# Kernel tuning notes

Hardware: AMD Instinct MI355X
Metric: run time of the kernel (lower is better)

## Reference

```python
import jax, jax.numpy as jnp
import numpy as np

B, S, D = 4, 2048, 1024

def setup_inputs() -> dict:
    key = jax.random.key(0)
    k0, k1, k2, k3 = jax.random.split(key, 4)
    scale = 1.0 / np.sqrt(D)
    return {
        "x": jax.random.normal(k0, (B, S, D), dtype=jnp.float32),
        "Wq": jax.random.normal(k1, (D, D), dtype=jnp.float32) * scale,
        "Wk": jax.random.normal(k2, (D, D), dtype=jnp.float32) * scale,
        "Wv": jax.random.normal(k3, (D, D), dtype=jnp.float32) * scale,
    }

def reference(x, Wq, Wk, Wv):
    # x: [B,S,D]; Wq/Wk/Wv: [D_in, D_out] (equivalent to torch Linear weight transposed)
    q = jnp.einsum('bsd,de->bse', x, Wq)
    k = jnp.einsum('bsd,de->bse', x, Wk)
    v = jnp.einsum('bsd,de->bse', x, Wv)
    d_out = k.shape[-1]
    scores = jnp.einsum('bqe,bke->bqk', q, k)  # [B,S,S]
    S_ = scores.shape[-1]
    causal = jnp.tril(jnp.ones((S_, S_), dtype=bool))  # True = keep
    # masked_fill before scaling == after scaling (-inf invariant under positive scale)
    scores = jnp.where(causal, scores, -jnp.inf)
    attn = jax.nn.softmax(scores / jnp.sqrt(jnp.asarray(d_out, scores.dtype)), axis=-1)
    # dropout p=0.0 -> identity
    return jnp.einsum('bqk,bke->bqe', attn, v)
```

## Files before the change

### kernel.cpp

```cpp
#include <hip/hip_runtime.h>

#define B_  4
#define S_  2048
#define D_  1024
#define N_  (B_*S_)
#define SCALE 0.03125f
#define NEGINF (-3.0e38f)

typedef unsigned short u16;
typedef __attribute__((ext_vector_type(8))) short short8;
typedef __attribute__((ext_vector_type(4))) float floatx4;

__device__ __forceinline__ u16 f2bf(float f) {
    unsigned int u = __float_as_uint(f);
    u += 0x7FFFu + ((u >> 16) & 1u);
    return (u16)(u >> 16);
}
__device__ __forceinline__ float bf2f(u16 h) {
    return __uint_as_float((unsigned int)h << 16);
}

__device__ __forceinline__ void gl_lds16(const void* g, void* l) {
    __builtin_amdgcn_global_load_lds(
        (const __attribute__((address_space(1))) unsigned int*)g,
        (__attribute__((address_space(3))) unsigned int*)l, 16, 0, 0);
}

__device__ __forceinline__ int xcd_chunk(int bid, int nwg) {
    return (bid & 7) * (nwg >> 3) + (bid >> 3);
}

__global__ __launch_bounds__(256) void cast_fused(const float* __restrict__ x,
                                                  const float* __restrict__ Wq, const float* __restrict__ Wk,
                                                  const float* __restrict__ Wv,
                                                  u16* __restrict__ xb, u16* __restrict__ Wqb,
                                                  u16* __restrict__ Wkb, u16* __restrict__ Wvt) {
    __shared__ float t[32][33];
    const int blk = blockIdx.x;
    if (blk < 5120) {
        const float* src; u16* dst; size_t i;
        if (blk < 4096)      { src = x;  dst = xb;  i = (size_t)blk * 2048; }
        else if (blk < 4608) { src = Wq; dst = Wqb; i = (size_t)(blk - 4096) * 2048; }
        else                 { src = Wk; dst = Wkb; i = (size_t)(blk - 4608) * 2048; }
        i += (size_t)threadIdx.x * 8;
        float4 a = *(const float4*)&src[i];
        float4 b = *(const float4*)&src[i + 4];
        short8 o;
        o[0]=f2bf(a.x); o[1]=f2bf(a.y); o[2]=f2bf(a.z); o[3]=f2bf(a.w);
        o[4]=f2bf(b.x); o[5]=f2bf(b.y); o[6]=f2bf(b.z); o[7]=f2bf(b.w);
        *(short8*)&dst[i] = o;
    } else {
        const int tb = blk - 5120;
        const int c = threadIdx.x & 31, r0 = threadIdx.x >> 5;
        const int i0 = (tb >> 5) * 32, j0 = (tb & 31) * 32;
#pragma unroll
        for (int rr = 0; rr < 4; ++rr)
            t[r0 + rr * 8][c] = Wv[(size_t)(i0 + r0 + rr * 8) * D_ + j0 + c];
        __syncthreads();
#pragma unroll
        for (int rr = 0; rr < 4; ++rr)
            Wvt[(size_t)(j0 + r0 + rr * 8) * D_ + i0 + c] = f2bf(t[c][r0 + rr * 8]);
    }
}


__device__ __forceinline__ void mfma_nt_128(const u16* __restrict__ A, int lda,
                                            const u16* __restrict__ Bp, int ldb,
                                            int m0, int n0, int kext,
                                            u16* Sh, floatx4 acc[4][4])
{
    const int tid  = threadIdx.x;
    const int lane = tid & 63;
    const int lr   = lane & 15, quad = lane >> 4;
    const int wm   = ((tid >> 6) & 1) * 64, wn = (tid >> 7) * 64;
    const int nt   = kext >> 6;

    auto stage8 = [&](int t) {
#pragma unroll
        for (int h = 0; h < 8; ++h) {
            const int kk = h >> 2, mat = (h >> 1) & 1, half = h & 1;
            const int idx = tid * 8;
            const int row = half * 64 + (idx >> 5);
            const int s   = (idx & 31) >> 3;
            const int gk  = (t << 6) + kk * 32 + ((s ^ ((row >> 1) & 3)) << 3);
            u16* dst = Sh + (t & 1) * 16384 + mat * 8192 + kk * 4096 + half * 2048 + idx;
            const u16* src = mat ? &Bp[(size_t)(n0 + row) * ldb + gk]
                                 : &A [(size_t)(m0 + row) * lda + gk];
            gl_lds16(src, dst);
        }
    };

    stage8(0);
    for (int t = 0; t < nt; ++t) {
        asm volatile("s_waitcnt vmcnt(0)" ::: "memory");
        __builtin_amdgcn_s_barrier();
        if (t + 1 < nt) stage8(t + 1);
        const u16* buf = Sh + (t & 1) * 16384;
#pragma unroll
        for (int kk = 0; kk < 2; ++kk) {
            short8 af[4], bf[4];
#pragma unroll
            for (int i = 0; i < 4; ++i) {
                const int ar = wm + i * 16 + lr;
                af[i] = *(const short8*)&buf[kk * 4096 + ar * 32 + ((quad ^ ((ar >> 1) & 3)) << 3)];
                const int br = wn + i * 16 + lr;
                bf[i] = *(const short8*)&buf[8192 + kk * 4096 + br * 32 + ((quad ^ ((br >> 1) & 3)) << 3)];
            }
            __builtin_amdgcn_s_setprio(1);
#pragma unroll
            for (int i = 0; i < 4; ++i)
#pragma unroll
                for (int j = 0; j < 4; ++j)
                    acc[i][j] = __builtin_amdgcn_mfma_f32_16x16x32_bf16(af[i], bf[j], acc[i][j], 0, 0, 0);
            __builtin_amdgcn_s_setprio(0);
        }
    }
}

#define EPI_VARS                                              \
    const int lane = threadIdx.x & 63;                        \
    const int lr = lane & 15, quad = lane >> 4;               \
    const int wm = ((threadIdx.x >> 6) & 1) * 64, wn = (threadIdx.x >> 7) * 64;

__device__ __forceinline__ void mfma_nt_128w8(const u16* __restrict__ A, int lda,
                                              const u16* __restrict__ Bp, int ldb,
                                              int m0, int n0, int kext,
                                              u16* Sh, floatx4 acc[2][4])
{
    const int tid  = threadIdx.x;
    const int lane = tid & 63;
    const int lr   = lane & 15, quad = lane >> 4;
    const int wid  = tid >> 6;
    const int wm   = (wid >> 1) * 32;
    const int wn   = (wid & 1) * 64;
    const int nt   = kext >> 6;

    auto stage4 = [&](int t) {
#pragma unroll
        for (int h = 0; h < 4; ++h) {
            const int kk = h >> 1, mat = h & 1;
            const int idx = tid * 8;
            const int row = idx >> 5;
            const int s   = (idx & 31) >> 3;
            const int gk  = (t << 6) + kk * 32 + ((s ^ ((row >> 1) & 3)) << 3);
            u16* dst = Sh + (t & 1) * 16384 + mat * 8192 + kk * 4096 + idx;
            const u16* src = mat ? &Bp[(size_t)(n0 + row) * ldb + gk]
                                 : &A [(size_t)(m0 + row) * lda + gk];
            gl_lds16(src, dst);
        }
    };

    stage4(0);
    for (int t = 0; t < nt; ++t) {
        asm volatile("s_waitcnt vmcnt(0)" ::: "memory");
        __builtin_amdgcn_s_barrier();
        if (t + 1 < nt) stage4(t + 1);
        const u16* buf = Sh + (t & 1) * 16384;
#pragma unroll
        for (int kk = 0; kk < 2; ++kk) {
            short8 af[2], bf[4];
#pragma unroll
            for (int i = 0; i < 2; ++i) {
                const int ar = wm + i * 16 + lr;
                af[i] = *(const short8*)&buf[kk * 4096 + ar * 32 + ((quad ^ ((ar >> 1) & 3)) << 3)];
            }
#pragma unroll
            for (int j = 0; j < 4; ++j) {
                const int br = wn + j * 16 + lr;
                bf[j] = *(const short8*)&buf[8192 + kk * 4096 + br * 32 + ((quad ^ ((br >> 1) & 3)) << 3)];
            }
            __builtin_amdgcn_s_setprio(1);
#pragma unroll
            for (int i = 0; i < 2; ++i)
#pragma unroll
                for (int j = 0; j < 4; ++j)
                    acc[i][j] = __builtin_amdgcn_mfma_f32_16x16x32_bf16(af[i], bf[j], acc[i][j], 0, 0, 0);
            __builtin_amdgcn_s_setprio(0);
        }
    }
}

__device__ __forceinline__ void mfma_nt_256(const u16* __restrict__ A, int lda,
                                            const u16* __restrict__ Bp, int ldb,
                                            int m0, int n0, int kext,
                                            u16* Sh, floatx4 acc[8][4])
{
    const int tid  = threadIdx.x;
    const int lane = tid & 63;
    const int lr   = lane & 15, quad = lane >> 4;
    const int wr   = (tid >> 8) & 1, wc = (tid >> 6) & 3;
    const int nt   = kext >> 6;

    auto stage8 = [&](int t) {
#pragma unroll
        for (int h = 0; h < 8; ++h) {
            const int kk = h >> 2, mat = (h >> 1) & 1, half = h & 1;
            const int idx = tid * 8;
            const int row = half * 128 + (idx >> 5);
            const int s   = (idx & 31) >> 3;
            const int gk  = (t << 6) + kk * 32 + ((s ^ ((row >> 1) & 3)) << 3);
            u16* dst = Sh + (t & 1) * 32768 + mat * 16384 + kk * 8192 + half * 4096 + idx;
            const u16* src = mat ? &Bp[(size_t)(n0 + row) * ldb + gk]
                                 : &A [(size_t)(m0 + row) * lda + gk];
            gl_lds16(src, dst);
        }
    };

    stage8(0);
    for (int t = 0; t < nt; ++t) {
        asm volatile("s_waitcnt vmcnt(0)" ::: "memory");
        __builtin_amdgcn_s_barrier();
        if (t + 1 < nt) stage8(t + 1);
        const u16* buf = Sh + (t & 1) * 32768;
#pragma unroll
        for (int kk = 0; kk < 2; ++kk) {
            short8 af[8], bf[4];
#pragma unroll
            for (int i = 0; i < 8; ++i) {
                const int ar = wr * 128 + i * 16 + lr;
                af[i] = *(const short8*)&buf[kk * 8192 + ar * 32 + ((quad ^ ((ar >> 1) & 3)) << 3)];
            }
#pragma unroll
            for (int j = 0; j < 4; ++j) {
                const int br = wc * 64 + j * 16 + lr;
                bf[j] = *(const short8*)&buf[16384 + kk * 8192 + br * 32 + ((quad ^ ((br >> 1) & 3)) << 3)];
            }
            __builtin_amdgcn_s_setprio(1);
#pragma unroll
            for (int i = 0; i < 8; ++i)
#pragma unroll
                for (int j = 0; j < 4; ++j)
                    acc[i][j] = __builtin_amdgcn_mfma_f32_16x16x32_bf16(af[i], bf[j], acc[i][j], 0, 0, 0);
            __builtin_amdgcn_s_setprio(0);
        }
    }
}

#define EPI256_VARS                                           \
    const int lane = threadIdx.x & 63;                        \
    const int lr = lane & 15, quad = lane >> 4;               \
    const int wr = (threadIdx.x >> 8) & 1, wc = (threadIdx.x >> 6) & 3;

__global__ __launch_bounds__(256) void mt_mfma(const u16* __restrict__ Wkb, const u16* __restrict__ Wqb,
                                               u16* __restrict__ Mt)
{
    __shared__ u16 Sh[32768];
    const int m0 = blockIdx.y * 128, n0 = blockIdx.x * 128;
    floatx4 acc[4][4];
#pragma unroll
    for (int i = 0; i < 4; ++i)
#pragma unroll
        for (int j = 0; j < 4; ++j) acc[i][j] = (floatx4){0.f, 0.f, 0.f, 0.f};
    mfma_nt_128(Wkb, D_, Wqb, D_, m0, n0, D_, Sh, acc);

    EPI_VARS
#pragma unroll
    for (int i = 0; i < 4; ++i)
#pragma unroll
        for (int j = 0; j < 4; ++j)
#pragma unroll
            for (int r = 0; r < 4; ++r)
                Mt[(size_t)(m0 + wm + i * 16 + quad * 4 + r) * D_ + n0 + wn + j * 16 + lr] = f2bf(acc[i][j][r]);
}

__global__ __launch_bounds__(512, 2) void yv_mfma(const u16* __restrict__ xb, const u16* __restrict__ Mt,
                                                  const u16* __restrict__ Wvt,
                                                  u16* __restrict__ Y, u16* __restrict__ Vt)
{
    __shared__ u16 Sh[65536];
    const int lid = xcd_chunk(blockIdx.x, 256);
    floatx4 acc[8][4];
#pragma unroll
    for (int i = 0; i < 8; ++i)
#pragma unroll
        for (int j = 0; j < 4; ++j) acc[i][j] = (floatx4){0.f, 0.f, 0.f, 0.f};

    if (lid < 128) {
        const int m0 = (lid >> 2) * 256, n0 = (lid & 3) * 256;
        mfma_nt_256(xb, D_, Mt, D_, m0, n0, D_, Sh, acc);
        EPI256_VARS
#pragma unroll
        for (int i = 0; i < 8; ++i)
#pragma unroll
            for (int j = 0; j < 4; ++j)
#pragma unroll
                for (int r = 0; r < 4; ++r)
                    Y[(size_t)(m0 + wr * 128 + i * 16 + quad * 4 + r) * D_ + n0 + wc * 64 + j * 16 + lr]
                        = f2bf(acc[i][j][r]);
    } else {
        const int v = lid - 128;
        const int b = v >> 5;
        const int mloc = ((v >> 2) & 7) * 256;
        const int n0 = (v & 3) * 256;
        const int m0 = b * S_ + mloc;
        u16* Vb = Vt + (size_t)b * D_ * S_;
        mfma_nt_256(xb, D_, Wvt, D_, m0, n0, D_, Sh, acc);
        EPI256_VARS
#pragma unroll
        for (int i = 0; i < 8; ++i)
#pragma unroll
            for (int j = 0; j < 4; ++j) {
                const int ee = n0 + wc * 64 + j * 16 + lr;
                const int s4 = mloc + wr * 128 + i * 16 + quad * 4;
                ushort4 o;
                o.x = f2bf(acc[i][j][0]); o.y = f2bf(acc[i][j][1]);
                o.z = f2bf(acc[i][j][2]); o.w = f2bf(acc[i][j][3]);
                *(ushort4*)&Vb[(size_t)ee * S_ + s4] = o;
            }
    }
}

__global__ __launch_bounds__(512, 2) void scores_mfma(const u16* __restrict__ Y, const u16* __restrict__ xb,
                                                      u16* __restrict__ Sc)
{
    __shared__ u16 Sh[65536];
    const int lid = xcd_chunk(blockIdx.x, 144);
    const int b = lid / 36;
    const int t = lid - b * 36;
    int qt = 0;
    while ((qt + 1) * (qt + 2) / 2 <= t) ++qt;
    const int kt = t - qt * (qt + 1) / 2;

    const u16* A  = Y  + (size_t)b * S_ * D_;
    const u16* Bp = xb + (size_t)b * S_ * D_;
    u16* Sb = Sc + (size_t)b * S_ * S_;
    const int m0 = qt * 256, n0 = kt * 256;
    floatx4 acc[8][4];
#pragma unroll
    for (int i = 0; i < 8; ++i)
#pragma unroll
        for (int j = 0; j < 4; ++j) acc[i][j] = (floatx4){0.f, 0.f, 0.f, 0.f};
    mfma_nt_256(A, D_, Bp, D_, m0, n0, D_, Sh, acc);

    EPI256_VARS
#pragma unroll
    for (int i = 0; i < 8; ++i)
#pragma unroll
        for (int r = 0; r < 4; ++r) {
            const int grow = m0 + wr * 128 + i * 16 + quad * 4 + r;
#pragma unroll
            for (int j = 0; j < 4; ++j) {
                const int gcol = n0 + wc * 64 + j * 16 + lr;
                const float v = (gcol <= grow) ? acc[i][j][r] * SCALE : NEGINF;
                Sb[(size_t)grow * S_ + gcol] = f2bf(v);
            }
        }
}

__global__ __launch_bounds__(256) void softmax_k(const u16* __restrict__ Sc, u16* __restrict__ P)
{
    const int row = blockIdx.x * 4 + (threadIdx.x >> 6);
    const int lane = threadIdx.x & 63;
    const int b = row >> 11, q = row & (S_ - 1);
    const int L = ((q >> 7) + 1) << 7;
    const u16* rp = Sc + ((size_t)b * S_ + q) * S_;
    u16* pp = P + ((size_t)b * S_ + q) * S_;

    float f[4][8];
    float lmax = -3.4e38f;
#pragma unroll
    for (int c = 0; c < 4; ++c) {
        const int i = c * 512 + lane * 8;
        if (i < L) {
            short8 v = *(const short8*)&rp[i];
#pragma unroll
            for (int k = 0; k < 8; ++k) { f[c][k] = bf2f((u16)v[k]); lmax = fmaxf(lmax, f[c][k]); }
        }
    }
#pragma unroll
    for (int off = 32; off; off >>= 1) lmax = fmaxf(lmax, __shfl_xor(lmax, off, 64));

    float lsum = 0.f;
#pragma unroll
    for (int c = 0; c < 4; ++c) {
        const int i = c * 512 + lane * 8;
        if (i < L) {
#pragma unroll
            for (int k = 0; k < 8; ++k) { f[c][k] = __expf(f[c][k] - lmax); lsum += f[c][k]; }
        }
    }
#pragma unroll
    for (int off = 32; off; off >>= 1) lsum += __shfl_xor(lsum, off, 64);
    const float inv = 1.0f / lsum;

#pragma unroll
    for (int c = 0; c < 4; ++c) {
        const int i = c * 512 + lane * 8;
        if (i < L) {
            short8 o;
#pragma unroll
            for (int k = 0; k < 8; ++k) o[k] = (short)f2bf(f[c][k] * inv);
            *(short8*)&pp[i] = o;
        }
    }
}

__device__ __forceinline__ void pv_epi(floatx4 acc[2][4], int b, int m0, int n0, float* __restrict__ O)
{
    const int lane = threadIdx.x & 63;
    const int lr = lane & 15, quad = lane >> 4;
    const int wid = threadIdx.x >> 6;
    const int wm = (wid >> 1) * 32, wn = (wid & 1) * 64;
#pragma unroll
    for (int i = 0; i < 2; ++i)
#pragma unroll
        for (int r = 0; r < 4; ++r) {
            const int grow = m0 + wm + i * 16 + quad * 4 + r;
#pragma unroll
            for (int j = 0; j < 4; ++j)
                O[((size_t)b * S_ + grow) * D_ + n0 + wn + j * 16 + lr] = acc[i][j][r];
        }
}

__global__ __launch_bounds__(512, 2) void pv_mfma(const u16* __restrict__ P, const u16* __restrict__ Vt,
                                                  float* __restrict__ O)
{
    __shared__ u16 Sh[32768];
    const int lid = xcd_chunk(blockIdx.x, 256);
    const int b  = lid >> 6;
    const int et = (lid >> 3) & 7;
    const int pr = lid & 7;
    const int n0 = et * 128;
    const u16* A  = P  + (size_t)b * S_ * S_;
    const u16* Bp = Vt + (size_t)b * D_ * S_;

    floatx4 acc[2][4];
    const int qtA = pr, qtB = 15 - pr;

#pragma unroll
    for (int i = 0; i < 2; ++i)
#pragma unroll
        for (int j = 0; j < 4; ++j) acc[i][j] = (floatx4){0.f, 0.f, 0.f, 0.f};
    mfma_nt_128w8(A, S_, Bp, S_, qtA * 128, n0, (qtA + 1) * 128, Sh, acc);
    pv_epi(acc, b, qtA * 128, n0, O);

#pragma unroll
    for (int i = 0; i < 2; ++i)
#pragma unroll
        for (int j = 0; j < 4; ++j) acc[i][j] = (floatx4){0.f, 0.f, 0.f, 0.f};
    mfma_nt_128w8(A, S_, Bp, S_, qtB * 128, n0, (qtB + 1) * 128, Sh, acc);
    pv_epi(acc, b, qtB * 128, n0, O);
}

extern "C" void kernel_launch(void* const* d_in, const int* in_sizes, int n_in,
                              void* d_out, int out_size, void* d_ws, size_t ws_size,
                              hipStream_t stream) {
    const float* x  = (const float*)d_in[0];
    const float* Wq = (const float*)d_in[1];
    const float* Wk = (const float*)d_in[2];
    const float* Wv = (const float*)d_in[3];
    float* out = (float*)d_out;
    char* w = (char*)d_ws;

    u16* xb  = (u16*)(w);
    u16* Wqb = (u16*)(w + 16777216);
    u16* Wkb = (u16*)(w + 18874368);
    u16* Wvt = (u16*)(w + 20971520);
    u16* Mt  = (u16*)(w + 23068672);
    u16* Y   = (u16*)(w + 25165824);
    u16* Vt  = (u16*)(w + 41943040);
    u16* Sc  = (u16*)(w + 58720256);
    u16* P   = (u16*)(w + 92274688);

    cast_fused <<<dim3(6144),   256, 0, stream>>>(x, Wq, Wk, Wv, xb, Wqb, Wkb, Wvt);
    mt_mfma    <<<dim3(8, 8),   256, 0, stream>>>(Wkb, Wqb, Mt);
    yv_mfma    <<<dim3(256),    512, 0, stream>>>(xb, Mt, Wvt, Y, Vt);
    scores_mfma<<<dim3(144),    512, 0, stream>>>(Y, xb, Sc);
    softmax_k  <<<dim3(N_/4),   256, 0, stream>>>(Sc, P);
    pv_mfma    <<<dim3(256),    512, 0, stream>>>(P, Vt, out);
}
```

Before: 211.0 us.

## Interleave per-slice global-to-LDS prefetch with MFMA half-tiles in 256x256 NT GEMM

Restructures the 256-wide NT GEMM main loop into a finer-grained ping-pong schedule. The next tile's loads are split into four A/B k-slices issued between half-tile MFMA phases, and partial vmcnt waits replace the full drain at each iteration. A-fragment registers are halved by processing the 8 row-fragments in two groups of four. The goal is to overlap global-to-LDS traffic with matrix math and cut register pressure, at the cost of many more barriers per iteration and fragile waitcnt accounting.

```diff
diff --git a/kernel.cpp b/kernel.cpp
--- a/kernel.cpp
+++ b/kernel.cpp
@@ -191,47 +191,77 @@
     const int wr   = (tid >> 8) & 1, wc = (tid >> 6) & 3;
     const int nt   = kext >> 6;
 
-    auto stage8 = [&](int t) {
-#pragma unroll
-        for (int h = 0; h < 8; ++h) {
-            const int kk = h >> 2, mat = (h >> 1) & 1, half = h & 1;
-            const int idx = tid * 8;
-            const int row = half * 128 + (idx >> 5);
+    auto stage = [&](int t, int mat, int kk) {
+#pragma unroll
+        for (int pass = 0; pass < 2; ++pass) {
+            const int idx = pass * 4096 + tid * 8;
+            const int row = idx >> 5;
             const int s   = (idx & 31) >> 3;
             const int gk  = (t << 6) + kk * 32 + ((s ^ ((row >> 1) & 3)) << 3);
-            u16* dst = Sh + (t & 1) * 32768 + mat * 16384 + kk * 8192 + half * 4096 + idx;
+            u16* dst = Sh + (t & 1) * 32768 + mat * 16384 + kk * 8192 + idx;
             const u16* src = mat ? &Bp[(size_t)(n0 + row) * ldb + gk]
                                  : &A [(size_t)(m0 + row) * lda + gk];
             gl_lds16(src, dst);
         }
     };
 
-    stage8(0);
+    stage(0, 0, 0); stage(0, 1, 0); stage(0, 0, 1); stage(0, 1, 1);
+    asm volatile("s_waitcnt vmcnt(4)" ::: "memory");
+    __builtin_amdgcn_s_barrier();
+
     for (int t = 0; t < nt; ++t) {
-        asm volatile("s_waitcnt vmcnt(0)" ::: "memory");
-        __builtin_amdgcn_s_barrier();
-        if (t + 1 < nt) stage8(t + 1);
         const u16* buf = Sh + (t & 1) * 32768;
+        const bool pf = (t + 1 < nt);
+        short8 af[4], bf[4];
+
 #pragma unroll
         for (int kk = 0; kk < 2; ++kk) {
-            short8 af[8], bf[4];
-#pragma unroll
-            for (int i = 0; i < 8; ++i) {
+            const int kb = kk * 8192;
+
+#pragma unroll
+            for (int i = 0; i < 4; ++i) {
                 const int ar = wr * 128 + i * 16 + lr;
-                af[i] = *(const short8*)&buf[kk * 8192 + ar * 32 + ((quad ^ ((ar >> 1) & 3)) << 3)];
+                af[i] = *(const short8*)&buf[kb + ar * 32 + ((quad ^ ((ar >> 1) & 3)) << 3)];
             }
 #pragma unroll
             for (int j = 0; j < 4; ++j) {
                 const int br = wc * 64 + j * 16 + lr;
-                bf[j] = *(const short8*)&buf[16384 + kk * 8192 + br * 32 + ((quad ^ ((br >> 1) & 3)) << 3)];
-            }
+                bf[j] = *(const short8*)&buf[16384 + kb + br * 32 + ((quad ^ ((br >> 1) & 3)) << 3)];
+            }
+            if (pf) stage(t + 1, 0, kk);
+            __builtin_amdgcn_s_barrier();
+            asm volatile("s_waitcnt lgkmcnt(0)" ::: "memory");
             __builtin_amdgcn_s_setprio(1);
 #pragma unroll
-            for (int i = 0; i < 8; ++i)
+            for (int i = 0; i < 4; ++i)
 #pragma unroll
                 for (int j = 0; j < 4; ++j)
                     acc[i][j] = __builtin_amdgcn_mfma_f32_16x16x32_bf16(af[i], bf[j], acc[i][j], 0, 0, 0);
             __builtin_amdgcn_s_setprio(0);
+            __builtin_amdgcn_s_barrier();
+
+#pragma unroll
+            for (int i = 0; i < 4; ++i) {
+                const int ar = wr * 128 + 64 + i * 16 + lr;
+                af[i] = *(const short8*)&buf[kb + ar * 32 + ((quad ^ ((ar >> 1) & 3)) << 3)];
+            }
+            if (pf) stage(t + 1, 1, kk);
+            if (kk == 0) {
+                if (pf) asm volatile("s_waitcnt vmcnt(4)" ::: "memory");
+                else    asm volatile("s_waitcnt vmcnt(0)" ::: "memory");
+            } else if (pf) {
+                asm volatile("s_waitcnt vmcnt(4)" ::: "memory");
+            }
+            __builtin_amdgcn_s_barrier();
+            asm volatile("s_waitcnt lgkmcnt(0)" ::: "memory");
+            __builtin_amdgcn_s_setprio(1);
+#pragma unroll
+            for (int i = 0; i < 4; ++i)
+#pragma unroll
+                for (int j = 0; j < 4; ++j)
+                    acc[4 + i][j] = __builtin_amdgcn_mfma_f32_16x16x32_bf16(af[i], bf[j], acc[4 + i][j], 0, 0, 0);
+            __builtin_amdgcn_s_setprio(0);
+            __builtin_amdgcn_s_barrier();
         }
     }
 }
```

Result: no change. 209.9 us (-0.5%).

## Switch projection and score GEMMs to 128x128 tiles, one tile per PV block

Applied to the files above, without the earlier changes.

The 256x256 tile GEMM path is replaced by the existing 128x128 eight-wave path for the Y/V projection and the causal scores kernel. Grids grow from 256 and 144 blocks to 1024 and 544, which fills more of the GPU's compute units. The PV kernel now gives each block a single q-tile instead of a paired short and long one, using 512 blocks with interleaved short and long tiles for load balance. The trade-off is lower data reuse per tile (more global and L2 traffic per flop) and more blocks to schedule. The causal masking in scores now skips work at 128-row granularity, which is finer than before.

```diff
diff --git a/kernel.cpp b/kernel.cpp
--- a/kernel.cpp
+++ b/kernel.cpp
@@ -180,66 +180,11 @@
     }
 }
 
-__device__ __forceinline__ void mfma_nt_256(const u16* __restrict__ A, int lda,
-                                            const u16* __restrict__ Bp, int ldb,
-                                            int m0, int n0, int kext,
-                                            u16* Sh, floatx4 acc[8][4])
-{
-    const int tid  = threadIdx.x;
-    const int lane = tid & 63;
-    const int lr   = lane & 15, quad = lane >> 4;
-    const int wr   = (tid >> 8) & 1, wc = (tid >> 6) & 3;
-    const int nt   = kext >> 6;
-
-    auto stage8 = [&](int t) {
-#pragma unroll
-        for (int h = 0; h < 8; ++h) {
-            const int kk = h >> 2, mat = (h >> 1) & 1, half = h & 1;
-            const int idx = tid * 8;
-            const int row = half * 128 + (idx >> 5);
-            const int s   = (idx & 31) >> 3;
-            const int gk  = (t << 6) + kk * 32 + ((s ^ ((row >> 1) & 3)) << 3);
-            u16* dst = Sh + (t & 1) * 32768 + mat * 16384 + kk * 8192 + half * 4096 + idx;
-            const u16* src = mat ? &Bp[(size_t)(n0 + row) * ldb + gk]
-                                 : &A [(size_t)(m0 + row) * lda + gk];
-            gl_lds16(src, dst);
-        }
-    };
-
-    stage8(0);
-    for (int t = 0; t < nt; ++t) {
-        asm volatile("s_waitcnt vmcnt(0)" ::: "memory");
-        __builtin_amdgcn_s_barrier();
-        if (t + 1 < nt) stage8(t + 1);
-        const u16* buf = Sh + (t & 1) * 32768;
-#pragma unroll
-        for (int kk = 0; kk < 2; ++kk) {
-            short8 af[8], bf[4];
-#pragma unroll
-            for (int i = 0; i < 8; ++i) {
-                const int ar = wr * 128 + i * 16 + lr;
-                af[i] = *(const short8*)&buf[kk * 8192 + ar * 32 + ((quad ^ ((ar >> 1) & 3)) << 3)];
-            }
-#pragma unroll
-            for (int j = 0; j < 4; ++j) {
-                const int br = wc * 64 + j * 16 + lr;
-                bf[j] = *(const short8*)&buf[16384 + kk * 8192 + br * 32 + ((quad ^ ((br >> 1) & 3)) << 3)];
-            }
-            __builtin_amdgcn_s_setprio(1);
-#pragma unroll
-            for (int i = 0; i < 8; ++i)
-#pragma unroll
-                for (int j = 0; j < 4; ++j)
-                    acc[i][j] = __builtin_amdgcn_mfma_f32_16x16x32_bf16(af[i], bf[j], acc[i][j], 0, 0, 0);
-            __builtin_amdgcn_s_setprio(0);
-        }
-    }
-}
-
-#define EPI256_VARS                                           \
+#define EPIW8_VARS                                            \
     const int lane = threadIdx.x & 63;                        \
     const int lr = lane & 15, quad = lane >> 4;               \
-    const int wr = (threadIdx.x >> 8) & 1, wc = (threadIdx.x >> 6) & 3;
+    const int wid = threadIdx.x >> 6;                         \
+    const int wm = (wid >> 1) * 32, wn = (wid & 1) * 64;
 
 __global__ __launch_bounds__(256) void mt_mfma(const u16* __restrict__ Wkb, const u16* __restrict__ Wqb,
                                                u16* __restrict__ Mt)
@@ -267,41 +212,41 @@
                                                   const u16* __restrict__ Wvt,
                                                   u16* __restrict__ Y, u16* __restrict__ Vt)
 {
-    __shared__ u16 Sh[65536];
-    const int lid = xcd_chunk(blockIdx.x, 256);
-    floatx4 acc[8][4];
-#pragma unroll
-    for (int i = 0; i < 8; ++i)
+    __shared__ u16 Sh[32768];
+    const int lid = xcd_chunk(blockIdx.x, 1024);
+    floatx4 acc[2][4];
+#pragma unroll
+    for (int i = 0; i < 2; ++i)
 #pragma unroll
         for (int j = 0; j < 4; ++j) acc[i][j] = (floatx4){0.f, 0.f, 0.f, 0.f};
 
-    if (lid < 128) {
-        const int m0 = (lid >> 2) * 256, n0 = (lid & 3) * 256;
-        mfma_nt_256(xb, D_, Mt, D_, m0, n0, D_, Sh, acc);
-        EPI256_VARS
-#pragma unroll
-        for (int i = 0; i < 8; ++i)
+    if (lid < 512) {
+        const int m0 = (lid >> 3) * 128, n0 = (lid & 7) * 128;
+        mfma_nt_128w8(xb, D_, Mt, D_, m0, n0, D_, Sh, acc);
+        EPIW8_VARS
+#pragma unroll
+        for (int i = 0; i < 2; ++i)
 #pragma unroll
             for (int j = 0; j < 4; ++j)
 #pragma unroll
                 for (int r = 0; r < 4; ++r)
-                    Y[(size_t)(m0 + wr * 128 + i * 16 + quad * 4 + r) * D_ + n0 + wc * 64 + j * 16 + lr]
+                    Y[(size_t)(m0 + wm + i * 16 + quad * 4 + r) * D_ + n0 + wn + j * 16 + lr]
                         = f2bf(acc[i][j][r]);
     } else {
-        const int v = lid - 128;
-        const int b = v >> 5;
-        const int mloc = ((v >> 2) & 7) * 256;
-        const int n0 = (v & 3) * 256;
+        const int v = lid - 512;
+        const int b = v >> 7;
+        const int mloc = ((v >> 3) & 15) * 128;
+        const int n0 = (v & 7) * 128;
         const int m0 = b * S_ + mloc;
         u16* Vb = Vt + (size_t)b * D_ * S_;
-        mfma_nt_256(xb, D_, Wvt, D_, m0, n0, D_, Sh, acc);
-        EPI256_VARS
-#pragma unroll
-        for (int i = 0; i < 8; ++i)
+        mfma_nt_128w8(xb, D_, Wvt, D_, m0, n0, D_, Sh, acc);
+        EPIW8_VARS
+#pragma unroll
+        for (int i = 0; i < 2; ++i)
 #pragma unroll
             for (int j = 0; j < 4; ++j) {
-                const int ee = n0 + wc * 64 + j * 16 + lr;
-                const int s4 = mloc + wr * 128 + i * 16 + quad * 4;
+                const int ee = n0 + wn + j * 16 + lr;
+                const int s4 = mloc + wm + i * 16 + quad * 4;
                 ushort4 o;
                 o.x = f2bf(acc[i][j][0]); o.y = f2bf(acc[i][j][1]);
                 o.z = f2bf(acc[i][j][2]); o.w = f2bf(acc[i][j][3]);
@@ -313,34 +258,35 @@
 __global__ __launch_bounds__(512, 2) void scores_mfma(const u16* __restrict__ Y, const u16* __restrict__ xb,
                                                       u16* __restrict__ Sc)
 {
-    __shared__ u16 Sh[65536];
-    const int lid = xcd_chunk(blockIdx.x, 144);
-    const int b = lid / 36;
-    const int t = lid - b * 36;
-    int qt = 0;
+    __shared__ u16 Sh[32768];
+    const int lid = xcd_chunk(blockIdx.x, 544);
+    const int b = lid / 136;
+    const int t = lid - b * 136;
+    int qt = (int)((sqrtf(8.0f * t + 1.0f) - 1.0f) * 0.5f);
     while ((qt + 1) * (qt + 2) / 2 <= t) ++qt;
+    while (qt * (qt + 1) / 2 > t) --qt;
     const int kt = t - qt * (qt + 1) / 2;
 
     const u16* A  = Y  + (size_t)b * S_ * D_;
     const u16* Bp = xb + (size_t)b * S_ * D_;
     u16* Sb = Sc + (size_t)b * S_ * S_;
-    const int m0 = qt * 256, n0 = kt * 256;
-    floatx4 acc[8][4];
-#pragma unroll
-    for (int i = 0; i < 8; ++i)
+    const int m0 = qt * 128, n0 = kt * 128;
+    floatx4 acc[2][4];
+#pragma unroll
+    for (int i = 0; i < 2; ++i)
 #pragma unroll
         for (int j = 0; j < 4; ++j) acc[i][j] = (floatx4){0.f, 0.f, 0.f, 0.f};
-    mfma_nt_256(A, D_, Bp, D_, m0, n0, D_, Sh, acc);
-
-    EPI256_VARS
-#pragma unroll
-    for (int i = 0; i < 8; ++i)
+    mfma_nt_128w8(A, D_, Bp, D_, m0, n0, D_, Sh, acc);
+
+    EPIW8_VARS
+#pragma unroll
+    for (int i = 0; i < 2; ++i)
 #pragma unroll
         for (int r = 0; r < 4; ++r) {
-            const int grow = m0 + wr * 128 + i * 16 + quad * 4 + r;
+            const int grow = m0 + wm + i * 16 + quad * 4 + r;
 #pragma unroll
             for (int j = 0; j < 4; ++j) {
-                const int gcol = n0 + wc * 64 + j * 16 + lr;
+                const int gcol = n0 + wn + j * 16 + lr;
                 const float v = (gcol <= grow) ? acc[i][j][r] * SCALE : NEGINF;
                 Sb[(size_t)grow * S_ + gcol] = f2bf(v);
             }
@@ -395,12 +341,28 @@
     }
 }
 
-__device__ __forceinline__ void pv_epi(floatx4 acc[2][4], int b, int m0, int n0, float* __restrict__ O)
-{
-    const int lane = threadIdx.x & 63;
-    const int lr = lane & 15, quad = lane >> 4;
-    const int wid = threadIdx.x >> 6;
-    const int wm = (wid >> 1) * 32, wn = (wid & 1) * 64;
+__global__ __launch_bounds__(512, 2) void pv_mfma(const u16* __restrict__ P, const u16* __restrict__ Vt,
+                                                  float* __restrict__ O)
+{
+    __shared__ u16 Sh[32768];
+    const int lid = xcd_chunk(blockIdx.x, 512);
+    const int s  = lid >> 5;
+    const int be = lid & 31;
+    const int b  = be >> 3, et = be & 7;
+    const int qt = (s & 1) ? 15 - (s >> 1) : (s >> 1);
+    const int m0 = qt * 128, n0 = et * 128;
+    const int kext = (qt + 1) * 128;
+    const u16* A  = P  + (size_t)b * S_ * S_;
+    const u16* Bp = Vt + (size_t)b * D_ * S_;
+
+    floatx4 acc[2][4];
+#pragma unroll
+    for (int i = 0; i < 2; ++i)
+#pragma unroll
+        for (int j = 0; j < 4; ++j) acc[i][j] = (floatx4){0.f, 0.f, 0.f, 0.f};
+    mfma_nt_128w8(A, S_, Bp, S_, m0, n0, kext, Sh, acc);
+
+    EPIW8_VARS
 #pragma unroll
     for (int i = 0; i < 2; ++i)
 #pragma unroll
@@ -410,36 +372,6 @@
             for (int j = 0; j < 4; ++j)
                 O[((size_t)b * S_ + grow) * D_ + n0 + wn + j * 16 + lr] = acc[i][j][r];
         }
-}
-
-__global__ __launch_bounds__(512, 2) void pv_mfma(const u16* __restrict__ P, const u16* __restrict__ Vt,
-                                                  float* __restrict__ O)
-{
-    __shared__ u16 Sh[32768];
-    const int lid = xcd_chunk(blockIdx.x, 256);
-    const int b  = lid >> 6;
-    const int et = (lid >> 3) & 7;
-    const int pr = lid & 7;
-    const int n0 = et * 128;
-    const u16* A  = P  + (size_t)b * S_ * S_;
-    const u16* Bp = Vt + (size_t)b * D_ * S_;
-
-    floatx4 acc[2][4];
-    const int qtA = pr, qtB = 15 - pr;
-
-#pragma unroll
-    for (int i = 0; i < 2; ++i)
-#pragma unroll
-        for (int j = 0; j < 4; ++j) acc[i][j] = (floatx4){0.f, 0.f, 0.f, 0.f};
-    mfma_nt_128w8(A, S_, Bp, S_, qtA * 128, n0, (qtA + 1) * 128, Sh, acc);
-    pv_epi(acc, b, qtA * 128, n0, O);
-
-#pragma unroll
-    for (int i = 0; i < 2; ++i)
-#pragma unroll
-        for (int j = 0; j < 4; ++j) acc[i][j] = (floatx4){0.f, 0.f, 0.f, 0.f};
-    mfma_nt_128w8(A, S_, Bp, S_, qtB * 128, n0, (qtB + 1) * 128, Sh, acc);
-    pv_epi(acc, b, qtB * 128, n0, O);
 }
 
 extern "C" void kernel_launch(void* const* d_in, const int* in_sizes, int n_in,
@@ -464,8 +396,8 @@
 
     cast_fused <<<dim3(6144),   256, 0, stream>>>(x, Wq, Wk, Wv, xb, Wqb, Wkb, Wvt);
     mt_mfma    <<<dim3(8, 8),   256, 0, stream>>>(Wkb, Wqb, Mt);
-    yv_mfma    <<<dim3(256),    512, 0, stream>>>(xb, Mt, Wvt, Y, Vt);
-    scores_mfma<<<dim3(144),    512, 0, stream>>>(Y, xb, Sc);
+    yv_mfma    <<<dim3(1024),   512, 0, stream>>>(xb, Mt, Wvt, Y, Vt);
+    scores_mfma<<<dim3(544),    512, 0, stream>>>(Y, xb, Sc);
     softmax_k  <<<dim3(N_/4),   256, 0, stream>>>(Sc, P);
-    pv_mfma    <<<dim3(256),    512, 0, stream>>>(P, Vt, out);
-}
+    pv_mfma    <<<dim3(512),    512, 0, stream>>>(P, Vt, out);
+}
```

Result: no change. 212.8 us (+0.9%).
